# Performance work log

Measured on AMD Instinct MI355X. Metric: run time of the kernel, lower is better.

## Reference

```python
import jax, jax.numpy as jnp
import numpy as np

B, D, K, E = 4096, 2048, 512, 8  # tokens, model dim, kept SVD rank, experts


def setup_inputs() -> dict:
    key = jax.random.key(0)
    ks = jax.random.split(key, 7)
    x = jax.random.normal(ks[0], (B, D), dtype=jnp.float32)
    # frozen base weight (stands in for pretrained_weight)
    W = jax.random.normal(ks[1], (D, D), dtype=jnp.float32) / np.sqrt(D)
    # frozen truncated SVD factors: U_k (D,K) left vecs, V_k (K,D) as sliced in the torch code
    U_k = jnp.linalg.qr(jax.random.normal(ks[2], (D, K), dtype=jnp.float32))[0]
    V_k = jnp.linalg.qr(jax.random.normal(ks[3], (D, K), dtype=jnp.float32))[0].T
    lambda_k = jax.random.normal(ks[4], (E, K), dtype=jnp.float32) * 0.02
    v = jnp.zeros((D,), dtype=jnp.float32)
    router_W1 = jax.random.normal(ks[5], (K, 1), dtype=jnp.float32)
    router_W2 = jax.random.normal(ks[6], (1, E), dtype=jnp.float32)
    return {"x": x, "W": W, "U_k": U_k, "V_k": V_k, "lambda_k": lambda_k,
            "v": v, "router_W1": router_W1, "router_W2": router_W2}


def reference(x, W, U_k, V_k, lambda_k, v, router_W1, router_W2):
    # routing: x @ U_k -> rank-1 router -> softmax over experts
    routing = x @ U_k                                   # (B,K)
    g = jax.nn.softmax((routing @ router_W1) @ router_W2, axis=-1)  # (B,E)
    # per-expert low-rank delta weight, materialized as in the original
    delta_W = jnp.einsum('dk,ek,kn->edn', U_k, lambda_k, V_k)       # (E,D,D)
    W_tot = W[None] + delta_W                           # (E,D,D)
    # F.linear semantics: out = x @ W_tot^T per expert
    expert_out = jnp.einsum('bd,end->ben', x, W_tot)    # (B,E,D)
    out = jnp.einsum('ben,be->bn', expert_out, g)       # gated combine
    return out * (1.0 + v)
```

## Files before the change

### kernel.cpp

```cpp
#include <hip/hip_runtime.h>
#include <hip/hip_bf16.h>
#include <cstdint>

#define B_TOK 4096
#define DDIM  2048
#define KR    512
#define NE    8

using f32x4  = __attribute__((ext_vector_type(4))) float;
using short8 = __attribute__((ext_vector_type(8))) short;
using u16 = unsigned short;

__device__ inline u16 f2bf(float f) {
    union { float f; uint32_t u; } x; x.f = f;
    uint32_t u = x.u;
    return (u16)((u + 0x7fffu + ((u >> 16) & 1u)) >> 16);
}
__device__ inline float bf2f(u16 h) {
    union { uint32_t u; float f; } x; x.u = ((uint32_t)h) << 16;
    return x.f;
}

__device__ inline void gload_lds16(const u16* g, u16* l) {
    __builtin_amdgcn_global_load_lds(
        (const __attribute__((address_space(1))) void*)g,
        (__attribute__((address_space(3))) void*)l, 16, 0, 0);
}

template<int COLS4, int SRC_LD, int DST_LD>
__device__ inline void cvt_region(const float* __restrict__ src,
                                  u16* __restrict__ dst, int i) {
    int r = i / COLS4, c = i - r * COLS4;
    float4 val = *((const float4*)(src + (size_t)r * SRC_LD) + c);
    ushort4 o;
    o.x = f2bf(val.x); o.y = f2bf(val.y); o.z = f2bf(val.z); o.w = f2bf(val.w);
    *(ushort4*)(dst + (size_t)r * DST_LD + c * 4) = o;
}

__global__ __launch_bounds__(256)
void prep_all(const float* __restrict__ x, const float* __restrict__ W,
              const float* __restrict__ U, const float* __restrict__ V,
              const float* __restrict__ W1,
              u16* __restrict__ Aaug, u16* __restrict__ BigB,
              u16* __restrict__ Vb, float* __restrict__ u1) {
    constexpr int NB_COPY = 1792;
    constexpr int N_X = 4096 * 512;
    constexpr int N_W = 2048 * 512;
    constexpr int N_U = 2048 * 128;
    constexpr int N_V = 512 * 512;
    constexpr int N_TOT = N_X + N_W + N_U + N_V;
    int b = blockIdx.x;
    if (b < NB_COPY) {
        for (int i = b * 256 + threadIdx.x; i < N_TOT; i += NB_COPY * 256) {
            if (i < N_X)                cvt_region<512, 2048, 2560>(x, Aaug, i);
            else if (i < N_X + N_W)     cvt_region<512, 2048, 2560>(W, BigB, i - N_X);
            else if (i < N_X + N_W + N_U)
                cvt_region<128, 512, 2560>(U, BigB + 2048, i - N_X - N_W);
            else                        cvt_region<512, 2048, 2048>(V, Vb, i - N_X - N_W - N_U);
        }
    } else {
        int wrow = (b - NB_COPY) * 4 + (threadIdx.x >> 6);
        int lane = threadIdx.x & 63;
        const float* row = U + (size_t)wrow * KR;
        float s = 0.f;
        #pragma unroll
        for (int k = 0; k < KR; k += 64) s += row[k + lane] * W1[k + lane];
        #pragma unroll
        for (int o = 32; o > 0; o >>= 1) s += __shfl_down(s, o);
        if (lane == 0) u1[wrow] = s;
    }
}

__global__ __launch_bounds__(256)
void router2(const u16* __restrict__ Ax, const float* __restrict__ u1,
             const float* __restrict__ W2, const float* __restrict__ lam,
             const float* __restrict__ tmat, u16* __restrict__ Am) {
    int b = blockIdx.x, tid = threadIdx.x;
    const u16* xr = Ax + (size_t)b * 2560;

    short8 xv = *(const short8*)(xr + tid * 8);
    float4 ua = *((const float4*)(u1 + tid * 8));
    float4 ub = *((const float4*)(u1 + tid * 8) + 1);
    float p = bf2f((u16)xv[0]) * ua.x + bf2f((u16)xv[1]) * ua.y +
              bf2f((u16)xv[2]) * ua.z + bf2f((u16)xv[3]) * ua.w +
              bf2f((u16)xv[4]) * ub.x + bf2f((u16)xv[5]) * ub.y +
              bf2f((u16)xv[6]) * ub.z + bf2f((u16)xv[7]) * ub.w;
    #pragma unroll
    for (int o = 32; o > 0; o >>= 1) p += __shfl_down(p, o);
    __shared__ float sp4[4];
    __shared__ float sbc;
    if ((tid & 63) == 0) sp4[tid >> 6] = p;
    __syncthreads();
    if (tid == 0) sbc = sp4[0] + sp4[1] + sp4[2] + sp4[3];
    __syncthreads();
    float s = sbc;

    float g[NE]; float mx = -1e30f;
    #pragma unroll
    for (int e = 0; e < NE; e++) { g[e] = s * W2[e]; mx = fmaxf(mx, g[e]); }
    float den = 0.f;
    #pragma unroll
    for (int e = 0; e < NE; e++) { g[e] = expf(g[e] - mx); den += g[e]; }
    float inv = 1.0f / den;

    for (int kk = tid; kk < KR; kk += 256) {
        float mu = 0.f;
        #pragma unroll
        for (int e = 0; e < NE; e++) mu += g[e] * lam[e * KR + kk];
        Am[(size_t)b * 2560 + 2048 + kk] =
            f2bf(mu * inv * tmat[(size_t)b * KR + kk]);
    }
}

template<int BM, int BN, int WGM, int WGN, bool HAS_V>
__global__ __launch_bounds__(256, 2)
void gemm_db(const u16* __restrict__ A, const u16* __restrict__ Bm,
             float* __restrict__ C, const float* __restrict__ v,
             int N, int Kc, int lda, int ldb, int nbx) {
    constexpr int MF = BM / (WGM * 16);
    constexpr int NF = BN / (WGN * 16);
    constexpr int ISSA = BM / 32;
    constexpr int ISSB = BN / 32;
    __shared__ u16 sA[2 * BM * 64];
    __shared__ u16 sB[2 * BN * 64];

    const int tid = threadIdx.x;
    const int wid = tid >> 6, lane = tid & 63;
    const int l15 = lane & 15, l4 = lane >> 4;
    const int wm = wid / WGN, wn = wid % WGN;

    const int nwg = gridDim.x;
    const int id = (blockIdx.x & 7) * (nwg >> 3) + (blockIdx.x >> 3);
    const int row0 = (id / nbx) * BM;
    const int col0 = (id % nbx) * BN;

    const int srow = tid >> 3;
    const int scol = ((tid & 7) ^ (srow & 7)) << 3;
    const u16* gA = A + (size_t)(row0 + srow) * lda + scol;
    const u16* gB = Bm + (size_t)(col0 + srow) * ldb + scol;

    f32x4 acc[MF][NF] = {};
    const int nt = Kc >> 6;

    #pragma unroll
    for (int i = 0; i < ISSA; i++)
        gload_lds16(gA + (size_t)i * 32 * lda, sA + i * 2048 + wid * 512);
    #pragma unroll
    for (int i = 0; i < ISSB; i++)
        gload_lds16(gB + (size_t)i * 32 * ldb, sB + i * 2048 + wid * 512);
    __syncthreads();

    for (int t = 0; t < nt; ++t) {
        const int cur = t & 1;
        if (t + 1 < nt) {
            const int nxt = cur ^ 1;
            const u16* gAk = gA + (size_t)(t + 1) * 64;
            const u16* gBk = gB + (size_t)(t + 1) * 64;
            #pragma unroll
            for (int i = 0; i < ISSA; i++)
                gload_lds16(gAk + (size_t)i * 32 * lda,
                            sA + nxt * BM * 64 + i * 2048 + wid * 512);
            #pragma unroll
            for (int i = 0; i < ISSB; i++)
                gload_lds16(gBk + (size_t)i * 32 * ldb,
                            sB + nxt * BN * 64 + i * 2048 + wid * 512);
        }
        const u16* a0 = sA + cur * BM * 64;
        const u16* b0 = sB + cur * BN * 64;
        #pragma unroll
        for (int kc = 0; kc < 8; kc += 4) {
            short8 af[MF], bv[NF];
            #pragma unroll
            for (int mf = 0; mf < MF; mf++) {
                int row = wm * MF * 16 + mf * 16 + l15;
                int ch = (kc + l4) ^ (row & 7);
                af[mf] = *(const short8*)(a0 + row * 64 + ch * 8);
            }
            #pragma unroll
            for (int nf = 0; nf < NF; nf++) {
                int row = wn * NF * 16 + nf * 16 + l15;
                int ch = (kc + l4) ^ (row & 7);
                bv[nf] = *(const short8*)(b0 + row * 64 + ch * 8);
            }
            #pragma unroll
            for (int mf = 0; mf < MF; mf++)
                #pragma unroll
                for (int nf = 0; nf < NF; nf++)
                    acc[mf][nf] = __builtin_amdgcn_mfma_f32_16x16x32_bf16(
                        af[mf], bv[nf], acc[mf][nf], 0, 0, 0);
        }
        __syncthreads();
    }

    #pragma unroll
    for (int nf = 0; nf < NF; nf++) {
        int col = col0 + wn * NF * 16 + nf * 16 + l15;
        float sc = HAS_V ? (1.0f + v[col]) : 1.0f;
        #pragma unroll
        for (int mf = 0; mf < MF; mf++) {
            int row = row0 + wm * MF * 16 + mf * 16 + l4 * 4;
            #pragma unroll
            for (int r2 = 0; r2 < 4; r2++)
                C[(size_t)(row + r2) * N + col] = acc[mf][nf][r2] * sc;
        }
    }
}

template<int BM, int BN, int WGM, int WGN, bool HAS_V>
__global__ __launch_bounds__(WGM * WGN * 64, 1)
void gemm_ph(const u16* __restrict__ A, const u16* __restrict__ Bm,
             float* __restrict__ C, const float* __restrict__ v,
             int N, int Kc, int lda, int ldb, int nbx) {
    constexpr int NT = WGM * WGN * 64;
    constexpr int MF = BM / (WGM * 16);
    constexpr int NF = BN / (WGN * 16);
    constexpr int SLOT = (BM + BN) * 64;
    constexpr int ROWS = NT / 8;
    constexpr int ISSA = BM / ROWS;
    constexpr int ISSB = BN / ROWS;
    static_assert(ISSA + ISSB == 6, "vmcnt literals assume 6 loads/tile");
    __shared__ u16 lds[3 * SLOT];

    const int tid = threadIdx.x;
    const int wid = tid >> 6, lane = tid & 63;
    const int l15 = lane & 15, l4 = lane >> 4;
    const int wm = wid / WGN, wn = wid % WGN;

    const int nwg = gridDim.x;
    const int id = (blockIdx.x & 7) * (nwg >> 3) + (blockIdx.x >> 3);
    const int row0 = (id / nbx) * BM;
    const int col0 = (id % nbx) * BN;

    const int srow = tid >> 3;
    const int scol = ((tid & 7) ^ (srow & 7)) << 3;
    const u16* gA = A + (size_t)(row0 + srow) * lda + scol;
    const u16* gB = Bm + (size_t)(col0 + srow) * ldb + scol;

    f32x4 acc[MF][NF] = {};
    const int nt = Kc >> 6;

    #pragma unroll
    for (int p = 0; p < 2; p++) {
        const u16* gAt = gA + p * 64;
        const u16* gBt = gB + p * 64;
        u16* sl = lds + p * SLOT;
        #pragma unroll
        for (int i = 0; i < ISSA; i++)
            gload_lds16(gAt + (size_t)i * ROWS * lda,
                        sl + i * ROWS * 64 + wid * 512);
        #pragma unroll
        for (int i = 0; i < ISSB; i++)
            gload_lds16(gBt + (size_t)i * ROWS * ldb,
                        sl + BM * 64 + i * ROWS * 64 + wid * 512);
    }
    asm volatile("s_waitcnt vmcnt(6)" ::: "memory");
    __builtin_amdgcn_s_barrier();

    int sc = 0, sp = 2;
    for (int t = 0; t < nt; ++t) {
        const u16* a0 = lds + sc * SLOT;
        const u16* b0 = a0 + BM * 64;
        const u16* gAt = gA + (size_t)(t + 2) * 64;
        const u16* gBt = gB + (size_t)(t + 2) * 64;
        u16* sl = lds + sp * SLOT;
        const bool pf = (t + 2 < nt);

        short8 af[MF], bv[NF];
        #pragma unroll
        for (int mf = 0; mf < MF; mf++) {
            int row = wm * MF * 16 + mf * 16 + l15;
            int ch = l4 ^ (row & 7);
            af[mf] = *(const short8*)(a0 + row * 64 + ch * 8);
        }
        #pragma unroll
        for (int nf = 0; nf < NF; nf++) {
            int row = wn * NF * 16 + nf * 16 + l15;
            int ch = l4 ^ (row & 7);
            bv[nf] = *(const short8*)(b0 + row * 64 + ch * 8);
        }
        if (pf) {
            gload_lds16(gAt,                         sl + wid * 512);
            gload_lds16(gAt + (size_t)ROWS * lda,    sl + ROWS * 64 + wid * 512);
            gload_lds16(gAt + (size_t)2 * ROWS * lda, sl + 2 * ROWS * 64 + wid * 512);
        }
        __builtin_amdgcn_s_barrier();
        asm volatile("s_waitcnt lgkmcnt(0)" ::: "memory");
        __builtin_amdgcn_s_setprio(1);
        #pragma unroll
        for (int mf = 0; mf < MF; mf++)
            #pragma unroll
            for (int nf = 0; nf < NF; nf++)
                acc[mf][nf] = __builtin_amdgcn_mfma_f32_16x16x32_bf16(
                    af[mf], bv[nf], acc[mf][nf], 0, 0, 0);
        __builtin_amdgcn_s_setprio(0);
        __builtin_amdgcn_s_barrier();

        #pragma unroll
        for (int mf = 0; mf < MF; mf++) {
            int row = wm * MF * 16 + mf * 16 + l15;
            int ch = (4 + l4) ^ (row & 7);
            af[mf] = *(const short8*)(a0 + row * 64 + ch * 8);
        }
        #pragma unroll
        for (int nf = 0; nf < NF; nf++) {
            int row = wn * NF * 16 + nf * 16 + l15;
            int ch = (4 + l4) ^ (row & 7);
            bv[nf] = *(const short8*)(b0 + row * 64 + ch * 8);
        }
        if (pf) {
            gload_lds16(gAt + (size_t)3 * ROWS * lda, sl + 3 * ROWS * 64 + wid * 512);
            gload_lds16(gBt,                          sl + BM * 64 + wid * 512);
            gload_lds16(gBt + (size_t)ROWS * ldb,     sl + BM * 64 + ROWS * 64 + wid * 512);
        }
        __builtin_amdgcn_s_barrier();
        asm volatile("s_waitcnt lgkmcnt(0)" ::: "memory");
        __builtin_amdgcn_s_setprio(1);
        #pragma unroll
        for (int mf = 0; mf < MF; mf++)
            #pragma unroll
            for (int nf = 0; nf < NF; nf++)
                acc[mf][nf] = __builtin_amdgcn_mfma_f32_16x16x32_bf16(
                    af[mf], bv[nf], acc[mf][nf], 0, 0, 0);
        __builtin_amdgcn_s_setprio(0);

        const int rem = nt - 1 - t;
        if (rem == 0) break;
        if (rem >= 2) asm volatile("s_waitcnt vmcnt(6)" ::: "memory");
        else          asm volatile("s_waitcnt vmcnt(0)" ::: "memory");
        __builtin_amdgcn_s_barrier();
        sc = (sc == 2) ? 0 : sc + 1;
        sp = (sp == 2) ? 0 : sp + 1;
    }

    #pragma unroll
    for (int nf = 0; nf < NF; nf++) {
        int col = col0 + wn * NF * 16 + nf * 16 + l15;
        float sc2 = HAS_V ? (1.0f + v[col]) : 1.0f;
        #pragma unroll
        for (int mf = 0; mf < MF; mf++) {
            int row = row0 + wm * MF * 16 + mf * 16 + l4 * 4;
            #pragma unroll
            for (int r2 = 0; r2 < 4; r2++)
                C[(size_t)(row + r2) * N + col] = acc[mf][nf][r2] * sc2;
        }
    }
}

extern "C" void kernel_launch(void* const* d_in, const int* in_sizes, int n_in,
                              void* d_out, int out_size, void* d_ws, size_t ws_size,
                              hipStream_t stream) {
    const float* x   = (const float*)d_in[0];
    const float* W   = (const float*)d_in[1];
    const float* U   = (const float*)d_in[2];
    const float* V   = (const float*)d_in[3];
    const float* lam = (const float*)d_in[4];
    const float* v   = (const float*)d_in[5];
    const float* W1  = (const float*)d_in[6];
    const float* W2  = (const float*)d_in[7];
    float* out = (float*)d_out;

    char* ws = (char*)d_ws;
    u16*   Aaug = (u16*)ws;
    u16*   BigB = (u16*)(ws + 20971520);
    u16*   Vb   = (u16*)(ws + 31457280);
    float* tmat = (float*)(ws + 33554432);
    float* u1   = (float*)(ws + 41943040);

    prep_all<<<2304, 256, 0, stream>>>(x, W, U, V, W1, Aaug, BigB, Vb, u1);

    gemm_db<128, 64, 4, 1, false><<<256, 256, 0, stream>>>(
        Aaug, Vb, tmat, nullptr, 512, 2048, 2560, 2048, 8);

    router2<<<4096, 256, 0, stream>>>(Aaug, u1, W2, lam, tmat, Aaug);

    gemm_ph<256, 128, 4, 2, true><<<256, 512, 0, stream>>>(
        Aaug, BigB, out, v, 2048, 2560, 2560, 2560, 16);
}
```

Before: 101.9 us.

## Rewrite main GEMM with 4 waves and register double-buffered fragment loads

The main 256x128-tile GEMM drops from 8 waves (512 threads) to 4 waves (256 threads). Each wave now computes a 128x64 sub-tile (8x4 MFMA fragments) instead of 64x64. Fragment loads for the second k-half are issued before the first half's MFMAs, and the next tile's first-half fragments are loaded between MFMA batches. This cuts barriers per k-step from three to one and hides LDS latency behind matrix work. The cost is roughly double the accumulator and fragment registers per wave and half as many waves to hide latency.

```diff
diff --git a/kernel.cpp b/kernel.cpp
--- a/kernel.cpp
+++ b/kernel.cpp
@@ -206,139 +206,110 @@
     }
 }
 
-template<int BM, int BN, int WGM, int WGN, bool HAS_V>
-__global__ __launch_bounds__(WGM * WGN * 64, 1)
-void gemm_ph(const u16* __restrict__ A, const u16* __restrict__ Bm,
-             float* __restrict__ C, const float* __restrict__ v,
-             int N, int Kc, int lda, int ldb, int nbx) {
-    constexpr int NT = WGM * WGN * 64;
-    constexpr int MF = BM / (WGM * 16);
-    constexpr int NF = BN / (WGN * 16);
-    constexpr int SLOT = (BM + BN) * 64;
-    constexpr int ROWS = NT / 8;
-    constexpr int ISSA = BM / ROWS;
-    constexpr int ISSB = BN / ROWS;
-    static_assert(ISSA + ISSB == 6, "vmcnt literals assume 6 loads/tile");
+template<bool HAS_V>
+__global__ __launch_bounds__(256, 1)
+void gemm_pipe(const u16* __restrict__ A, const u16* __restrict__ Bm,
+               float* __restrict__ C, const float* __restrict__ v,
+               int N, int Kc, int lda, int ldb, int nbx) {
+    constexpr int SLOT = (256 + 128) * 64;
     __shared__ u16 lds[3 * SLOT];
 
     const int tid = threadIdx.x;
     const int wid = tid >> 6, lane = tid & 63;
     const int l15 = lane & 15, l4 = lane >> 4;
-    const int wm = wid / WGN, wn = wid % WGN;
+    const int wm = wid >> 1, wn = wid & 1;
 
     const int nwg = gridDim.x;
     const int id = (blockIdx.x & 7) * (nwg >> 3) + (blockIdx.x >> 3);
-    const int row0 = (id / nbx) * BM;
-    const int col0 = (id % nbx) * BN;
+    const int row0 = (id / nbx) * 256;
+    const int col0 = (id % nbx) * 128;
 
     const int srow = tid >> 3;
     const int scol = ((tid & 7) ^ (srow & 7)) << 3;
     const u16* gA = A + (size_t)(row0 + srow) * lda + scol;
     const u16* gB = Bm + (size_t)(col0 + srow) * ldb + scol;
-
-    f32x4 acc[MF][NF] = {};
+    const int lofs = wid * 512;
+
+    f32x4 acc[8][4] = {};
+    short8 a0f[8], b0f[4], a1f[8], b1f[4];
+
     const int nt = Kc >> 6;
 
-    #pragma unroll
-    for (int p = 0; p < 2; p++) {
-        const u16* gAt = gA + p * 64;
-        const u16* gBt = gB + p * 64;
-        u16* sl = lds + p * SLOT;
-        #pragma unroll
-        for (int i = 0; i < ISSA; i++)
-            gload_lds16(gAt + (size_t)i * ROWS * lda,
-                        sl + i * ROWS * 64 + wid * 512);
-        #pragma unroll
-        for (int i = 0; i < ISSB; i++)
-            gload_lds16(gBt + (size_t)i * ROWS * ldb,
-                        sl + BM * 64 + i * ROWS * 64 + wid * 512);
-    }
-    asm volatile("s_waitcnt vmcnt(6)" ::: "memory");
+    auto STAGE = [&](int t, int s) {
+        const u16* gAt = gA + (size_t)t * 64;
+        const u16* gBt = gB + (size_t)t * 64;
+        u16* sl = lds + s * SLOT;
+        #pragma unroll
+        for (int i = 0; i < 8; i++)
+            gload_lds16(gAt + (size_t)i * 32 * lda, sl + i * 2048 + lofs);
+        #pragma unroll
+        for (int i = 0; i < 4; i++)
+            gload_lds16(gBt + (size_t)i * 32 * ldb, sl + 16384 + i * 2048 + lofs);
+    };
+    auto LDA_ = [&](short8 (&af)[8], const u16* base, int kc) {
+        #pragma unroll
+        for (int mf = 0; mf < 8; mf++) {
+            int row = wm * 128 + mf * 16 + l15;
+            int ch = (kc + l4) ^ (row & 7);
+            af[mf] = *(const short8*)(base + row * 64 + ch * 8);
+        }
+    };
+    auto LDB_ = [&](short8 (&bf)[4], const u16* base, int kc) {
+        #pragma unroll
+        for (int nf = 0; nf < 4; nf++) {
+            int row = wn * 64 + nf * 16 + l15;
+            int ch = (kc + l4) ^ (row & 7);
+            bf[nf] = *(const short8*)(base + row * 64 + ch * 8);
+        }
+    };
+    auto MM = [&](short8 (&af)[8], short8 (&bf)[4]) {
+        __builtin_amdgcn_s_setprio(1);
+        #pragma unroll
+        for (int mf = 0; mf < 8; mf++)
+            #pragma unroll
+            for (int nf = 0; nf < 4; nf++)
+                acc[mf][nf] = __builtin_amdgcn_mfma_f32_16x16x32_bf16(
+                    af[mf], bf[nf], acc[mf][nf], 0, 0, 0);
+        __builtin_amdgcn_s_setprio(0);
+    };
+
+    STAGE(0, 0);
+    STAGE(1, 1);
+    asm volatile("s_waitcnt vmcnt(12)" ::: "memory");
     __builtin_amdgcn_s_barrier();
-
-    int sc = 0, sp = 2;
+    asm volatile("" ::: "memory");
+    LDA_(a0f, lds, 0);
+    LDB_(b0f, lds + 16384, 0);
+
+    int sl_cur = 0;
     for (int t = 0; t < nt; ++t) {
-        const u16* a0 = lds + sc * SLOT;
-        const u16* b0 = a0 + BM * 64;
-        const u16* gAt = gA + (size_t)(t + 2) * 64;
-        const u16* gBt = gB + (size_t)(t + 2) * 64;
-        u16* sl = lds + sp * SLOT;
-        const bool pf = (t + 2 < nt);
-
-        short8 af[MF], bv[NF];
-        #pragma unroll
-        for (int mf = 0; mf < MF; mf++) {
-            int row = wm * MF * 16 + mf * 16 + l15;
-            int ch = l4 ^ (row & 7);
-            af[mf] = *(const short8*)(a0 + row * 64 + ch * 8);
-        }
-        #pragma unroll
-        for (int nf = 0; nf < NF; nf++) {
-            int row = wn * NF * 16 + nf * 16 + l15;
-            int ch = l4 ^ (row & 7);
-            bv[nf] = *(const short8*)(b0 + row * 64 + ch * 8);
-        }
-        if (pf) {
-            gload_lds16(gAt,                         sl + wid * 512);
-            gload_lds16(gAt + (size_t)ROWS * lda,    sl + ROWS * 64 + wid * 512);
-            gload_lds16(gAt + (size_t)2 * ROWS * lda, sl + 2 * ROWS * 64 + wid * 512);
-        }
-        __builtin_amdgcn_s_barrier();
-        asm volatile("s_waitcnt lgkmcnt(0)" ::: "memory");
-        __builtin_amdgcn_s_setprio(1);
-        #pragma unroll
-        for (int mf = 0; mf < MF; mf++)
-            #pragma unroll
-            for (int nf = 0; nf < NF; nf++)
-                acc[mf][nf] = __builtin_amdgcn_mfma_f32_16x16x32_bf16(
-                    af[mf], bv[nf], acc[mf][nf], 0, 0, 0);
-        __builtin_amdgcn_s_setprio(0);
-        __builtin_amdgcn_s_barrier();
-
-        #pragma unroll
-        for (int mf = 0; mf < MF; mf++) {
-            int row = wm * MF * 16 + mf * 16 + l15;
-            int ch = (4 + l4) ^ (row & 7);
-            af[mf] = *(const short8*)(a0 + row * 64 + ch * 8);
-        }
-        #pragma unroll
-        for (int nf = 0; nf < NF; nf++) {
-            int row = wn * NF * 16 + nf * 16 + l15;
-            int ch = (4 + l4) ^ (row & 7);
-            bv[nf] = *(const short8*)(b0 + row * 64 + ch * 8);
-        }
-        if (pf) {
-            gload_lds16(gAt + (size_t)3 * ROWS * lda, sl + 3 * ROWS * 64 + wid * 512);
-            gload_lds16(gBt,                          sl + BM * 64 + wid * 512);
-            gload_lds16(gBt + (size_t)ROWS * ldb,     sl + BM * 64 + ROWS * 64 + wid * 512);
-        }
-        __builtin_amdgcn_s_barrier();
-        asm volatile("s_waitcnt lgkmcnt(0)" ::: "memory");
-        __builtin_amdgcn_s_setprio(1);
-        #pragma unroll
-        for (int mf = 0; mf < MF; mf++)
-            #pragma unroll
-            for (int nf = 0; nf < NF; nf++)
-                acc[mf][nf] = __builtin_amdgcn_mfma_f32_16x16x32_bf16(
-                    af[mf], bv[nf], acc[mf][nf], 0, 0, 0);
-        __builtin_amdgcn_s_setprio(0);
-
-        const int rem = nt - 1 - t;
-        if (rem == 0) break;
-        if (rem >= 2) asm volatile("s_waitcnt vmcnt(6)" ::: "memory");
-        else          asm volatile("s_waitcnt vmcnt(0)" ::: "memory");
-        __builtin_amdgcn_s_barrier();
-        sc = (sc == 2) ? 0 : sc + 1;
-        sp = (sp == 2) ? 0 : sp + 1;
-    }
-
-    #pragma unroll
-    for (int nf = 0; nf < NF; nf++) {
-        int col = col0 + wn * NF * 16 + nf * 16 + l15;
+        const u16* sc_ = lds + sl_cur * SLOT;
+        if (t + 2 < nt) STAGE(t + 2, (sl_cur >= 1) ? sl_cur - 1 : sl_cur + 2);
+        LDA_(a1f, sc_, 4);
+        LDB_(b1f, sc_ + 16384, 4);
+        MM(a0f, b0f);
+        if (t + 1 < nt) {
+            asm volatile("" ::: "memory");
+            if (t + 2 < nt) asm volatile("s_waitcnt vmcnt(12)" ::: "memory");
+            else            asm volatile("s_waitcnt vmcnt(0)" ::: "memory");
+            __builtin_amdgcn_s_barrier();
+            asm volatile("" ::: "memory");
+            const int sl_nxt = (sl_cur == 2) ? 0 : sl_cur + 1;
+            const u16* sn_ = lds + sl_nxt * SLOT;
+            LDA_(a0f, sn_, 0);
+            LDB_(b0f, sn_ + 16384, 0);
+            sl_cur = sl_nxt;
+        }
+        MM(a1f, b1f);
+    }
+
+    #pragma unroll
+    for (int nf = 0; nf < 4; nf++) {
+        int col = col0 + wn * 64 + nf * 16 + l15;
         float sc2 = HAS_V ? (1.0f + v[col]) : 1.0f;
         #pragma unroll
-        for (int mf = 0; mf < MF; mf++) {
-            int row = row0 + wm * MF * 16 + mf * 16 + l4 * 4;
+        for (int mf = 0; mf < 8; mf++) {
+            int row = row0 + wm * 128 + mf * 16 + l4 * 4;
             #pragma unroll
             for (int r2 = 0; r2 < 4; r2++)
                 C[(size_t)(row + r2) * N + col] = acc[mf][nf][r2] * sc2;
@@ -373,6 +344,6 @@
 
     router2<<<4096, 256, 0, stream>>>(Aaug, u1, W2, lam, tmat, Aaug);
 
-    gemm_ph<256, 128, 4, 2, true><<<256, 512, 0, stream>>>(
+    gemm_pipe<true><<<256, 256, 0, stream>>>(
         Aaug, BigB, out, v, 2048, 2560, 2560, 2560, 16);
 }
```

New measurement: 114.3 us. 12.2% more time.
